# Kernel tuning notes

Hardware: AMD Instinct MI355X
Metric: run time of the kernel (lower is better)

Reference implementation:

```python
import jax, jax.numpy as jnp
import numpy as np

N_NODES = 50000
N_EDGES = 500000
D_NODE = 128
D_EDGE = 128
D_HID = 512
D_OUT = 128


def setup_inputs() -> dict:
    key = jax.random.key(0)
    ks = jax.random.split(key, 6)
    x = jax.random.normal(ks[0], (N_NODES, D_NODE), dtype=jnp.float32)
    edge_index = jax.random.randint(ks[1], (2, N_EDGES), 0, N_NODES, dtype=jnp.int64 if jax.config.jax_enable_x64 else jnp.int32)
    edge_attr = jax.random.normal(ks[2], (N_EDGES, D_EDGE), dtype=jnp.float32)
    cin = 2 * D_NODE + D_EDGE
    W1 = jax.random.normal(ks[3], (cin, D_HID), dtype=jnp.float32) * (1.0 / np.sqrt(cin))
    b1 = jnp.zeros((D_HID,), dtype=jnp.float32)
    W2 = jax.random.normal(ks[4], (D_HID, D_OUT), dtype=jnp.float32) * (1.0 / np.sqrt(D_HID))
    b2 = jnp.zeros((D_OUT,), dtype=jnp.float32)
    return {"x": x, "edge_index": edge_index, "edge_attr": edge_attr,
            "W1": W1, "b1": b1, "W2": W2, "b2": b2}


def reference(x, edge_index, edge_attr, W1, b1, W2, b2):
    row, col = edge_index[0], edge_index[1]
    source = x[row]            # [E, d_node] gather
    target = x[col]            # [E, d_node] gather
    out = jnp.concatenate([source, target, edge_attr], axis=1)  # [E, 2*d_node + d_edge]
    h = jax.nn.relu(out @ W1 + b1)   # [E, d_hid]
    return h @ W2 + b2               # [E, d_out]
```

## Files before the change

kernel.cpp:

```cpp
#include <hip/hip_runtime.h>

#define E_TOTAL 500000
#define N_NODES 50000
#define DN 128
#define CIN 384
#define DH 512
#define DOUT 128
#define MT 128
#define NTILE 3907
#define SA_ROWB 768
#define SH_ROWB 1024
#define SO_LD 132

typedef short short8 __attribute__((ext_vector_type(8)));
typedef float f32x4 __attribute__((ext_vector_type(4)));

__device__ inline short f2bf(float f) {
    unsigned int u = __float_as_uint(f);
    u = (u + 0x7FFFu + ((u >> 16) & 1u)) >> 16;
    return (short)u;
}

__global__ void prep_weights(const float* __restrict__ w1,
                             const float* __restrict__ w2,
                             short* __restrict__ w1t,
                             short* __restrict__ w2t) {
    __shared__ float t[32][33];
    int b = blockIdx.x;
    const float* src; short* dst; int R, C, tr, tc;
    if (b < 192) { src = w1; dst = w1t; R = 384; C = 512; tr = b >> 4; tc = b & 15; }
    else { b -= 192; src = w2; dst = w2t; R = 512; C = 128; tr = b >> 2; tc = b & 3; }
    int lx = threadIdx.x & 31, ly = threadIdx.x >> 5;
#pragma unroll
    for (int p = 0; p < 4; p++) {
        int r = tr * 32 + p * 8 + ly;
        t[p * 8 + ly][lx] = src[(size_t)r * C + tc * 32 + lx];
    }
    __syncthreads();
#pragma unroll
    for (int p = 0; p < 4; p++) {
        int c = tc * 32 + p * 8 + ly;
        dst[(size_t)c * R + tr * 32 + lx] = f2bf(t[lx][p * 8 + ly]);
    }
}

__global__ void cvt_x(const float* __restrict__ x, short* __restrict__ xb) {
    int i = blockIdx.x * 256 + threadIdx.x;
    const float4* s = reinterpret_cast<const float4*>(x) + (size_t)i * 2;
    float4 a = s[0], b = s[1];
    short8 p;
    p[0] = f2bf(a.x); p[1] = f2bf(a.y); p[2] = f2bf(a.z); p[3] = f2bf(a.w);
    p[4] = f2bf(b.x); p[5] = f2bf(b.y); p[6] = f2bf(b.z); p[7] = f2bf(b.w);
    reinterpret_cast<short8*>(xb)[i] = p;
}

__global__ __launch_bounds__(1024, 4) void edge_mlp(
        const short* __restrict__ xb,
        const float* __restrict__ xf,
        const int* __restrict__ ei,
        const float* __restrict__ ea,
        const float* __restrict__ b1,
        const float* __restrict__ b2,
        const short* __restrict__ w1t,
        const short* __restrict__ w2t,
        float* __restrict__ out) {
    __shared__ short sBuf[65536];
    __shared__ int sIdx[2][MT];
    char* sb = (char*)sBuf;

    const int tid = threadIdx.x;
    const int wave = tid >> 6;
    const int lane = tid & 63;
    const int l16 = lane & 15;
    const int quad = lane >> 4;
    const int lane32 = tid & 31;
    const int g = tid >> 5;
    const int xorv = (l16 & 7) << 4;
    const int e0 = blockIdx.x * MT;

    if (tid < 2 * MT) {
        int rr = tid >> 7, r = tid & 127;
        int e = e0 + r; e = e < E_TOTAL ? e : E_TOTAL - 1;
        sIdx[rr][r] = ei[rr * E_TOTAL + e];
    }
    __syncthreads();

    short4 gx[8];
    float4 ge[4];
    if (xb) {
#pragma unroll
        for (int j = 0; j < 4; j++) {
            int r = g + 32 * j;
            gx[j]     = reinterpret_cast<const short4*>(xb + (size_t)sIdx[0][r] * DN)[lane32];
            gx[4 + j] = reinterpret_cast<const short4*>(xb + (size_t)sIdx[1][r] * DN)[lane32];
            int e = e0 + r; e = e < E_TOTAL ? e : E_TOTAL - 1;
            ge[j] = reinterpret_cast<const float4*>(ea + (size_t)e * DN)[lane32];
        }
    } else {
#pragma unroll
        for (int j = 0; j < 4; j++) {
            int r = g + 32 * j;
            float4 v0 = reinterpret_cast<const float4*>(xf + (size_t)sIdx[0][r] * DN)[lane32];
            float4 v1 = reinterpret_cast<const float4*>(xf + (size_t)sIdx[1][r] * DN)[lane32];
            short4 p0, p1;
            p0.x = f2bf(v0.x); p0.y = f2bf(v0.y); p0.z = f2bf(v0.z); p0.w = f2bf(v0.w);
            p1.x = f2bf(v1.x); p1.y = f2bf(v1.y); p1.z = f2bf(v1.z); p1.w = f2bf(v1.w);
            gx[j] = p0; gx[4 + j] = p1;
            int e = e0 + r; e = e < E_TOTAL ? e : E_TOTAL - 1;
            ge[j] = reinterpret_cast<const float4*>(ea + (size_t)e * DN)[lane32];
        }
    }
    const short* base1 = w1t + (size_t)(wave * 32 + l16) * CIN + quad * 8;
    short8 bb[2];
#pragma unroll
    for (int nt = 0; nt < 2; nt++)
        bb[nt] = *reinterpret_cast<const short8*>(base1 + nt * 16 * CIN);
#pragma unroll
    for (int j = 0; j < 4; j++) {
        int r = g + 32 * j;
        int rx = (r & 7) << 4;
        char* row = sb + r * SA_ROWB;
        *reinterpret_cast<short4*>(row + (( 0 * 256 + lane32 * 8) ^ rx)) = gx[j];
        *reinterpret_cast<short4*>(row + (( 1 * 256 + lane32 * 8) ^ rx)) = gx[4 + j];
        short4 p;
        p.x = f2bf(ge[j].x); p.y = f2bf(ge[j].y); p.z = f2bf(ge[j].z); p.w = f2bf(ge[j].w);
        *reinterpret_cast<short4*>(row + (( 2 * 256 + lane32 * 8) ^ rx)) = p;
    }
    __syncthreads();

    f32x4 acc[2][8] = {};
    for (int k = 0; k < CIN; k += 32) {
        short8 bn[2];
        if (k + 32 < CIN) {
#pragma unroll
            for (int nt = 0; nt < 2; nt++)
                bn[nt] = *reinterpret_cast<const short8*>(base1 + nt * 16 * CIN + k + 32);
        }
        short8 a[8];
#pragma unroll
        for (int mt = 0; mt < 8; mt++) {
            int m = mt * 16 + l16;
            a[mt] = *reinterpret_cast<const short8*>(
                sb + m * SA_ROWB + ((2 * k + quad * 16) ^ xorv));
        }
#pragma unroll
        for (int nt = 0; nt < 2; nt++)
#pragma unroll
            for (int mt = 0; mt < 8; mt++)
                acc[nt][mt] = __builtin_amdgcn_mfma_f32_16x16x32_bf16(bb[nt], a[mt], acc[nt][mt], 0, 0, 0);
        if (k + 32 < CIN) {
#pragma unroll
            for (int nt = 0; nt < 2; nt++) bb[nt] = bn[nt];
        }
    }

    const int wn = wave & 7, half = wave >> 3;
    const short* base2 = w2t + (size_t)(wn * 16 + l16) * DH + quad * 8;
    short8 bw = *reinterpret_cast<const short8*>(base2);
    float4 b1v[2];
#pragma unroll
    for (int nt = 0; nt < 2; nt++)
        b1v[nt] = *reinterpret_cast<const float4*>(&b1[wave * 32 + nt * 16 + quad * 4]);

    __syncthreads();

#pragma unroll
    for (int nt = 0; nt < 2; nt++) {
#pragma unroll
        for (int mt = 0; mt < 8; mt++) {
            int m = mt * 16 + l16;
            short4 p;
            p.x = f2bf(fmaxf(acc[nt][mt][0] + b1v[nt].x, 0.0f));
            p.y = f2bf(fmaxf(acc[nt][mt][1] + b1v[nt].y, 0.0f));
            p.z = f2bf(fmaxf(acc[nt][mt][2] + b1v[nt].z, 0.0f));
            p.w = f2bf(fmaxf(acc[nt][mt][3] + b1v[nt].w, 0.0f));
            *reinterpret_cast<short4*>(
                sb + m * SH_ROWB + ((wave * 64 + nt * 32 + quad * 8) ^ xorv)) = p;
        }
    }
    __syncthreads();

    f32x4 acc2[4] = {};
#pragma unroll
    for (int kk = 0; kk < 16; kk++) {
        short8 bn = bw;
        if (kk < 15) bn = *reinterpret_cast<const short8*>(base2 + (kk + 1) * 32);
        short8 hf[4];
#pragma unroll
        for (int mt = 0; mt < 4; mt++) {
            int m = half * 64 + mt * 16 + l16;
            hf[mt] = *reinterpret_cast<const short8*>(
                sb + m * SH_ROWB + ((kk * 64 + quad * 16) ^ xorv));
        }
#pragma unroll
        for (int mt = 0; mt < 4; mt++)
            acc2[mt] = __builtin_amdgcn_mfma_f32_16x16x32_bf16(bw, hf[mt], acc2[mt], 0, 0, 0);
        bw = bn;
    }
    float4 b2v = *reinterpret_cast<const float4*>(&b2[wn * 16 + quad * 4]);
    __syncthreads();

    float (*sO)[SO_LD] = (float (*)[SO_LD])sBuf;
#pragma unroll
    for (int mt = 0; mt < 4; mt++) {
        int m = half * 64 + mt * 16 + l16;
        f32x4 o = acc2[mt];
        float* dst = &sO[m][wn * 16 + quad * 4];
        dst[0] = o[0] + b2v.x; dst[1] = o[1] + b2v.y;
        dst[2] = o[2] + b2v.z; dst[3] = o[3] + b2v.w;
    }
    __syncthreads();
#pragma unroll
    for (int it = 0; it < 4; it++) {
        int idx = tid + it * 1024;
        int row = idx >> 5, col = (idx & 31) * 4;
        int e = e0 + row;
        if (e < E_TOTAL) {
            float4 v = *reinterpret_cast<const float4*>(&sO[row][col]);
            *reinterpret_cast<float4*>(&out[(size_t)e * DOUT + col]) = v;
        }
    }
}

extern "C" void kernel_launch(void* const* d_in, const int* in_sizes, int n_in,
                              void* d_out, int out_size, void* d_ws, size_t ws_size,
                              hipStream_t stream) {
    const float* x  = (const float*)d_in[0];
    const int*   ei = (const int*)d_in[1];
    const float* ea = (const float*)d_in[2];
    const float* W1 = (const float*)d_in[3];
    const float* b1 = (const float*)d_in[4];
    const float* W2 = (const float*)d_in[5];
    const float* b2 = (const float*)d_in[6];
    float* outp = (float*)d_out;

    short* w1t = (short*)d_ws;
    short* w2t = w1t + DH * CIN;
    prep_weights<<<256, 256, 0, stream>>>(W1, W2, w1t, w2t);

    const size_t wt_bytes = (size_t)(DH * CIN + DOUT * DH) * 2;
    const size_t xb_bytes = (size_t)N_NODES * DN * 2;
    short* xbp = nullptr;
    if (ws_size >= wt_bytes + xb_bytes) {
        xbp = w2t + DOUT * DH;
        cvt_x<<<3125, 256, 0, stream>>>(x, xbp);
    }
    edge_mlp<<<NTILE, 1024, 0, stream>>>(xbp, x, ei, ea, b1, b2, w1t, w2t, outp);
}
```

Baseline: 941.7 us.

## Gather node features directly into LDS with global_load_lds and segmented layout

Replaces the register-staged gather of bf16 node rows with direct global-to-LDS loads (global_load_lds, 16 bytes per lane), using a segmented A-tile layout with a pre-swizzled source column so the XOR swizzle is kept. Edge indices are now loaded per lane instead of through a shared index array and a barrier. The weight prep and x conversion kernels are merged into one launch. The aim is to cut register pressure, LDS write instructions and one sync in the gather phase, at the cost of a more intricate layout and a templated duplicate code path.

```diff
diff --git a/kernel.cpp b/kernel.cpp
--- a/kernel.cpp
+++ b/kernel.cpp
@@ -8,7 +8,7 @@
 #define DOUT 128
 #define MT 128
 #define NTILE 3907
-#define SA_ROWB 768
+#define SEG_B 32768
 #define SH_ROWB 1024
 #define SO_LD 132
 
@@ -21,12 +21,30 @@
     return (short)u;
 }
 
-__global__ void prep_weights(const float* __restrict__ w1,
-                             const float* __restrict__ w2,
-                             short* __restrict__ w1t,
-                             short* __restrict__ w2t) {
+__device__ inline void gload16(const void* gsrc, void* ldst) {
+    __builtin_amdgcn_global_load_lds(
+        (const __attribute__((address_space(1))) unsigned int*)gsrc,
+        (__attribute__((address_space(3))) unsigned int*)ldst, 16, 0, 0);
+}
+
+__global__ void prep_all(const float* __restrict__ w1,
+                         const float* __restrict__ w2,
+                         const float* __restrict__ x,
+                         short* __restrict__ w1t,
+                         short* __restrict__ w2t,
+                         short* __restrict__ xb) {
     __shared__ float t[32][33];
     int b = blockIdx.x;
+    if (b >= 256) {
+        int i = (b - 256) * 256 + threadIdx.x;
+        const float4* s = reinterpret_cast<const float4*>(x) + (size_t)i * 2;
+        float4 a = s[0], c = s[1];
+        short8 p;
+        p[0] = f2bf(a.x); p[1] = f2bf(a.y); p[2] = f2bf(a.z); p[3] = f2bf(a.w);
+        p[4] = f2bf(c.x); p[5] = f2bf(c.y); p[6] = f2bf(c.z); p[7] = f2bf(c.w);
+        reinterpret_cast<short8*>(xb)[i] = p;
+        return;
+    }
     const float* src; short* dst; int R, C, tr, tc;
     if (b < 192) { src = w1; dst = w1t; R = 384; C = 512; tr = b >> 4; tc = b & 15; }
     else { b -= 192; src = w2; dst = w2t; R = 512; C = 128; tr = b >> 2; tc = b & 3; }
@@ -44,16 +62,7 @@
     }
 }
 
-__global__ void cvt_x(const float* __restrict__ x, short* __restrict__ xb) {
-    int i = blockIdx.x * 256 + threadIdx.x;
-    const float4* s = reinterpret_cast<const float4*>(x) + (size_t)i * 2;
-    float4 a = s[0], b = s[1];
-    short8 p;
-    p[0] = f2bf(a.x); p[1] = f2bf(a.y); p[2] = f2bf(a.z); p[3] = f2bf(a.w);
-    p[4] = f2bf(b.x); p[5] = f2bf(b.y); p[6] = f2bf(b.z); p[7] = f2bf(b.w);
-    reinterpret_cast<short8*>(xb)[i] = p;
-}
-
+template<int XB>
 __global__ __launch_bounds__(1024, 4) void edge_mlp(
         const short* __restrict__ xb,
         const float* __restrict__ xf,
@@ -65,7 +74,6 @@
         const short* __restrict__ w2t,
         float* __restrict__ out) {
     __shared__ short sBuf[65536];
-    __shared__ int sIdx[2][MT];
     char* sb = (char*)sBuf;
 
     const int tid = threadIdx.x;
@@ -73,151 +81,265 @@
     const int lane = tid & 63;
     const int l16 = lane & 15;
     const int quad = lane >> 4;
-    const int lane32 = tid & 31;
-    const int g = tid >> 5;
     const int xorv = (l16 & 7) << 4;
     const int e0 = blockIdx.x * MT;
 
-    if (tid < 2 * MT) {
-        int rr = tid >> 7, r = tid & 127;
-        int e = e0 + r; e = e < E_TOTAL ? e : E_TOTAL - 1;
-        sIdx[rr][r] = ei[rr * E_TOTAL + e];
-    }
-    __syncthreads();
-
-    short4 gx[8];
-    float4 ge[4];
-    if (xb) {
+    if (XB) {
+        int idxv[4];
 #pragma unroll
         for (int j = 0; j < 4; j++) {
-            int r = g + 32 * j;
-            gx[j]     = reinterpret_cast<const short4*>(xb + (size_t)sIdx[0][r] * DN)[lane32];
-            gx[4 + j] = reinterpret_cast<const short4*>(xb + (size_t)sIdx[1][r] * DN)[lane32];
+            int u = wave + j * 16;
+            int seg = u >> 5;
+            int r4 = (u & 31) * 4;
+            int e = e0 + r4 + (lane >> 4); e = e < E_TOTAL ? e : E_TOTAL - 1;
+            idxv[j] = ei[seg * E_TOTAL + e];
+        }
+        const int lane32 = lane & 31, rsel = lane >> 5;
+        float4 ge[4];
+#pragma unroll
+        for (int j = 0; j < 4; j++) {
+            int r = wave * 8 + j * 2 + rsel;
             int e = e0 + r; e = e < E_TOTAL ? e : E_TOTAL - 1;
             ge[j] = reinterpret_cast<const float4*>(ea + (size_t)e * DN)[lane32];
         }
-    } else {
 #pragma unroll
         for (int j = 0; j < 4; j++) {
-            int r = g + 32 * j;
-            float4 v0 = reinterpret_cast<const float4*>(xf + (size_t)sIdx[0][r] * DN)[lane32];
-            float4 v1 = reinterpret_cast<const float4*>(xf + (size_t)sIdx[1][r] * DN)[lane32];
-            short4 p0, p1;
-            p0.x = f2bf(v0.x); p0.y = f2bf(v0.y); p0.z = f2bf(v0.z); p0.w = f2bf(v0.w);
-            p1.x = f2bf(v1.x); p1.y = f2bf(v1.y); p1.z = f2bf(v1.z); p1.w = f2bf(v1.w);
-            gx[j] = p0; gx[4 + j] = p1;
-            int e = e0 + r; e = e < E_TOTAL ? e : E_TOTAL - 1;
-            ge[j] = reinterpret_cast<const float4*>(ea + (size_t)e * DN)[lane32];
-        }
-    }
-    const short* base1 = w1t + (size_t)(wave * 32 + l16) * CIN + quad * 8;
-    short8 bb[2];
-#pragma unroll
-    for (int nt = 0; nt < 2; nt++)
-        bb[nt] = *reinterpret_cast<const short8*>(base1 + nt * 16 * CIN);
-#pragma unroll
-    for (int j = 0; j < 4; j++) {
-        int r = g + 32 * j;
-        int rx = (r & 7) << 4;
-        char* row = sb + r * SA_ROWB;
-        *reinterpret_cast<short4*>(row + (( 0 * 256 + lane32 * 8) ^ rx)) = gx[j];
-        *reinterpret_cast<short4*>(row + (( 1 * 256 + lane32 * 8) ^ rx)) = gx[4 + j];
-        short4 p;
-        p.x = f2bf(ge[j].x); p.y = f2bf(ge[j].y); p.z = f2bf(ge[j].z); p.w = f2bf(ge[j].w);
-        *reinterpret_cast<short4*>(row + (( 2 * 256 + lane32 * 8) ^ rx)) = p;
-    }
-    __syncthreads();
-
-    f32x4 acc[2][8] = {};
-    for (int k = 0; k < CIN; k += 32) {
-        short8 bn[2];
-        if (k + 32 < CIN) {
+            int u = wave + j * 16;
+            int seg = u >> 5;
+            int r4 = (u & 31) * 4;
+            int row = r4 + (lane >> 4);
+            int lc = ((lane & 15) * 16) ^ ((row & 7) << 4);
+            const char* gsrc = (const char*)(xb + (size_t)idxv[j] * DN) + lc;
+            gload16(gsrc, sb + seg * SEG_B + r4 * 256);
+        }
+        const short* base1p = w1t + (size_t)(wave * 32 + l16) * CIN + quad * 8;
+        short8 bb0 = *reinterpret_cast<const short8*>(base1p);
+        short8 bb1 = *reinterpret_cast<const short8*>(base1p + 16 * CIN);
+#pragma unroll
+        for (int j = 0; j < 4; j++) {
+            int r = wave * 8 + j * 2 + rsel;
+            short4 p;
+            p.x = f2bf(ge[j].x); p.y = f2bf(ge[j].y); p.z = f2bf(ge[j].z); p.w = f2bf(ge[j].w);
+            int pc = (lane32 * 8) ^ ((r & 7) << 4);
+            *reinterpret_cast<short4*>(sb + 2 * SEG_B + r * 256 + pc) = p;
+        }
+        __syncthreads();
+
+        f32x4 acc[2][8] = {};
+        short8 bb[2] = {bb0, bb1};
+        for (int k = 0; k < CIN; k += 32) {
+            short8 bn[2];
+            if (k + 32 < CIN) {
+#pragma unroll
+                for (int nt = 0; nt < 2; nt++)
+                    bn[nt] = *reinterpret_cast<const short8*>(base1p + nt * 16 * CIN + k + 32);
+            }
+            int segb = (k >> 7) * SEG_B, kk2 = 2 * (k & 127);
+            short8 a[8];
+#pragma unroll
+            for (int mt = 0; mt < 8; mt++) {
+                int m = mt * 16 + l16;
+                a[mt] = *reinterpret_cast<const short8*>(
+                    sb + segb + m * 256 + ((kk2 + quad * 16) ^ xorv));
+            }
 #pragma unroll
             for (int nt = 0; nt < 2; nt++)
-                bn[nt] = *reinterpret_cast<const short8*>(base1 + nt * 16 * CIN + k + 32);
-        }
-        short8 a[8];
-#pragma unroll
-        for (int mt = 0; mt < 8; mt++) {
-            int m = mt * 16 + l16;
-            a[mt] = *reinterpret_cast<const short8*>(
-                sb + m * SA_ROWB + ((2 * k + quad * 16) ^ xorv));
-        }
+#pragma unroll
+                for (int mt = 0; mt < 8; mt++)
+                    acc[nt][mt] = __builtin_amdgcn_mfma_f32_16x16x32_bf16(bb[nt], a[mt], acc[nt][mt], 0, 0, 0);
+            if (k + 32 < CIN) { bb[0] = bn[0]; bb[1] = bn[1]; }
+        }
+
+        const int wn = wave & 7, half = wave >> 3;
+        const short* base2 = w2t + (size_t)(wn * 16 + l16) * DH + quad * 8;
+        short8 bw = *reinterpret_cast<const short8*>(base2);
+        float4 b1v[2];
 #pragma unroll
         for (int nt = 0; nt < 2; nt++)
-#pragma unroll
-            for (int mt = 0; mt < 8; mt++)
-                acc[nt][mt] = __builtin_amdgcn_mfma_f32_16x16x32_bf16(bb[nt], a[mt], acc[nt][mt], 0, 0, 0);
-        if (k + 32 < CIN) {
-#pragma unroll
-            for (int nt = 0; nt < 2; nt++) bb[nt] = bn[nt];
-        }
-    }
-
-    const int wn = wave & 7, half = wave >> 3;
-    const short* base2 = w2t + (size_t)(wn * 16 + l16) * DH + quad * 8;
-    short8 bw = *reinterpret_cast<const short8*>(base2);
-    float4 b1v[2];
-#pragma unroll
-    for (int nt = 0; nt < 2; nt++)
-        b1v[nt] = *reinterpret_cast<const float4*>(&b1[wave * 32 + nt * 16 + quad * 4]);
-
-    __syncthreads();
-
-#pragma unroll
-    for (int nt = 0; nt < 2; nt++) {
-#pragma unroll
-        for (int mt = 0; mt < 8; mt++) {
-            int m = mt * 16 + l16;
-            short4 p;
-            p.x = f2bf(fmaxf(acc[nt][mt][0] + b1v[nt].x, 0.0f));
-            p.y = f2bf(fmaxf(acc[nt][mt][1] + b1v[nt].y, 0.0f));
-            p.z = f2bf(fmaxf(acc[nt][mt][2] + b1v[nt].z, 0.0f));
-            p.w = f2bf(fmaxf(acc[nt][mt][3] + b1v[nt].w, 0.0f));
-            *reinterpret_cast<short4*>(
-                sb + m * SH_ROWB + ((wave * 64 + nt * 32 + quad * 8) ^ xorv)) = p;
-        }
-    }
-    __syncthreads();
-
-    f32x4 acc2[4] = {};
-#pragma unroll
-    for (int kk = 0; kk < 16; kk++) {
-        short8 bn = bw;
-        if (kk < 15) bn = *reinterpret_cast<const short8*>(base2 + (kk + 1) * 32);
-        short8 hf[4];
+            b1v[nt] = *reinterpret_cast<const float4*>(&b1[wave * 32 + nt * 16 + quad * 4]);
+        __syncthreads();
+
+#pragma unroll
+        for (int nt = 0; nt < 2; nt++) {
+#pragma unroll
+            for (int mt = 0; mt < 8; mt++) {
+                int m = mt * 16 + l16;
+                short4 p;
+                p.x = f2bf(fmaxf(acc[nt][mt][0] + b1v[nt].x, 0.0f));
+                p.y = f2bf(fmaxf(acc[nt][mt][1] + b1v[nt].y, 0.0f));
+                p.z = f2bf(fmaxf(acc[nt][mt][2] + b1v[nt].z, 0.0f));
+                p.w = f2bf(fmaxf(acc[nt][mt][3] + b1v[nt].w, 0.0f));
+                *reinterpret_cast<short4*>(
+                    sb + m * SH_ROWB + ((wave * 64 + nt * 32 + quad * 8) ^ xorv)) = p;
+            }
+        }
+        __syncthreads();
+
+        f32x4 acc2[4] = {};
+#pragma unroll
+        for (int kk = 0; kk < 16; kk++) {
+            short8 bn = bw;
+            if (kk < 15) bn = *reinterpret_cast<const short8*>(base2 + (kk + 1) * 32);
+            short8 hf[4];
+#pragma unroll
+            for (int mt = 0; mt < 4; mt++) {
+                int m = half * 64 + mt * 16 + l16;
+                hf[mt] = *reinterpret_cast<const short8*>(
+                    sb + m * SH_ROWB + ((kk * 64 + quad * 16) ^ xorv));
+            }
+#pragma unroll
+            for (int mt = 0; mt < 4; mt++)
+                acc2[mt] = __builtin_amdgcn_mfma_f32_16x16x32_bf16(bw, hf[mt], acc2[mt], 0, 0, 0);
+            bw = bn;
+        }
+        float4 b2v = *reinterpret_cast<const float4*>(&b2[wn * 16 + quad * 4]);
+        __syncthreads();
+
+        float (*sO)[SO_LD] = (float (*)[SO_LD])sBuf;
 #pragma unroll
         for (int mt = 0; mt < 4; mt++) {
             int m = half * 64 + mt * 16 + l16;
-            hf[mt] = *reinterpret_cast<const short8*>(
-                sb + m * SH_ROWB + ((kk * 64 + quad * 16) ^ xorv));
-        }
-#pragma unroll
-        for (int mt = 0; mt < 4; mt++)
-            acc2[mt] = __builtin_amdgcn_mfma_f32_16x16x32_bf16(bw, hf[mt], acc2[mt], 0, 0, 0);
-        bw = bn;
-    }
-    float4 b2v = *reinterpret_cast<const float4*>(&b2[wn * 16 + quad * 4]);
-    __syncthreads();
-
-    float (*sO)[SO_LD] = (float (*)[SO_LD])sBuf;
-#pragma unroll
-    for (int mt = 0; mt < 4; mt++) {
-        int m = half * 64 + mt * 16 + l16;
-        f32x4 o = acc2[mt];
-        float* dst = &sO[m][wn * 16 + quad * 4];
-        dst[0] = o[0] + b2v.x; dst[1] = o[1] + b2v.y;
-        dst[2] = o[2] + b2v.z; dst[3] = o[3] + b2v.w;
-    }
-    __syncthreads();
-#pragma unroll
-    for (int it = 0; it < 4; it++) {
-        int idx = tid + it * 1024;
-        int row = idx >> 5, col = (idx & 31) * 4;
-        int e = e0 + row;
-        if (e < E_TOTAL) {
-            float4 v = *reinterpret_cast<const float4*>(&sO[row][col]);
-            *reinterpret_cast<float4*>(&out[(size_t)e * DOUT + col]) = v;
+            float* dst = &sO[m][wn * 16 + quad * 4];
+            dst[0] = acc2[mt][0] + b2v.x; dst[1] = acc2[mt][1] + b2v.y;
+            dst[2] = acc2[mt][2] + b2v.z; dst[3] = acc2[mt][3] + b2v.w;
+        }
+        __syncthreads();
+#pragma unroll
+        for (int it = 0; it < 4; it++) {
+            int idx = tid + it * 1024;
+            int row = idx >> 5, col = (idx & 31) * 4;
+            int e = e0 + row;
+            if (e < E_TOTAL) {
+                float4 v = *reinterpret_cast<const float4*>(&sO[row][col]);
+                *reinterpret_cast<float4*>(&out[(size_t)e * DOUT + col]) = v;
+            }
+        }
+    } else {
+        int* sIdx = (int*)(sb + 122880);
+        if (tid < 2 * MT) {
+            int rr = tid >> 7, r = tid & 127;
+            int e = e0 + r; e = e < E_TOTAL ? e : E_TOTAL - 1;
+            sIdx[rr * MT + r] = ei[rr * E_TOTAL + e];
+        }
+        __syncthreads();
+        const int lane32 = lane & 31;
+        const int g = tid >> 5;
+#pragma unroll
+        for (int h2 = 0; h2 < 2; h2++) {
+            float4 v0[2], v1[2], ve[2];
+#pragma unroll
+            for (int jj = 0; jj < 2; jj++) {
+                int r = g + 32 * (h2 * 2 + jj);
+                v0[jj] = reinterpret_cast<const float4*>(xf + (size_t)sIdx[r] * DN)[lane32];
+                v1[jj] = reinterpret_cast<const float4*>(xf + (size_t)sIdx[MT + r] * DN)[lane32];
+                int e = e0 + r; e = e < E_TOTAL ? e : E_TOTAL - 1;
+                ve[jj] = reinterpret_cast<const float4*>(ea + (size_t)e * DN)[lane32];
+            }
+#pragma unroll
+            for (int jj = 0; jj < 2; jj++) {
+                int r = g + 32 * (h2 * 2 + jj);
+                int rx = (r & 7) << 4;
+                int pc0 = (lane32 & 15) * 16 + (lane32 >> 4) * 8;
+                (void)pc0;
+                int pc = (lane32 * 8) ^ rx;
+                short4 p0, p1, pe;
+                p0.x = f2bf(v0[jj].x); p0.y = f2bf(v0[jj].y); p0.z = f2bf(v0[jj].z); p0.w = f2bf(v0[jj].w);
+                p1.x = f2bf(v1[jj].x); p1.y = f2bf(v1[jj].y); p1.z = f2bf(v1[jj].z); p1.w = f2bf(v1[jj].w);
+                pe.x = f2bf(ve[jj].x); pe.y = f2bf(ve[jj].y); pe.z = f2bf(ve[jj].z); pe.w = f2bf(ve[jj].w);
+                *reinterpret_cast<short4*>(sb + 0 * SEG_B + r * 256 + pc) = p0;
+                *reinterpret_cast<short4*>(sb + 1 * SEG_B + r * 256 + pc) = p1;
+                *reinterpret_cast<short4*>(sb + 2 * SEG_B + r * 256 + pc) = pe;
+            }
+        }
+        const short* base1p = w1t + (size_t)(wave * 32 + l16) * CIN + quad * 8;
+        short8 bb0 = *reinterpret_cast<const short8*>(base1p);
+        short8 bb1 = *reinterpret_cast<const short8*>(base1p + 16 * CIN);
+        __syncthreads();
+
+        f32x4 acc[2][8] = {};
+        short8 bb[2] = {bb0, bb1};
+        for (int k = 0; k < CIN; k += 32) {
+            short8 bn[2];
+            if (k + 32 < CIN) {
+#pragma unroll
+                for (int nt = 0; nt < 2; nt++)
+                    bn[nt] = *reinterpret_cast<const short8*>(base1p + nt * 16 * CIN + k + 32);
+            }
+            int segb = (k >> 7) * SEG_B, kk2 = 2 * (k & 127);
+            short8 a[8];
+#pragma unroll
+            for (int mt = 0; mt < 8; mt++) {
+                int m = mt * 16 + l16;
+                a[mt] = *reinterpret_cast<const short8*>(
+                    sb + segb + m * 256 + ((kk2 + quad * 16) ^ xorv));
+            }
+#pragma unroll
+            for (int nt = 0; nt < 2; nt++)
+#pragma unroll
+                for (int mt = 0; mt < 8; mt++)
+                    acc[nt][mt] = __builtin_amdgcn_mfma_f32_16x16x32_bf16(bb[nt], a[mt], acc[nt][mt], 0, 0, 0);
+            if (k + 32 < CIN) { bb[0] = bn[0]; bb[1] = bn[1]; }
+        }
+        const int wn = wave & 7, half = wave >> 3;
+        const short* base2 = w2t + (size_t)(wn * 16 + l16) * DH + quad * 8;
+        short8 bw = *reinterpret_cast<const short8*>(base2);
+        float4 b1v[2];
+#pragma unroll
+        for (int nt = 0; nt < 2; nt++)
+            b1v[nt] = *reinterpret_cast<const float4*>(&b1[wave * 32 + nt * 16 + quad * 4]);
+        __syncthreads();
+#pragma unroll
+        for (int nt = 0; nt < 2; nt++) {
+#pragma unroll
+            for (int mt = 0; mt < 8; mt++) {
+                int m = mt * 16 + l16;
+                short4 p;
+                p.x = f2bf(fmaxf(acc[nt][mt][0] + b1v[nt].x, 0.0f));
+                p.y = f2bf(fmaxf(acc[nt][mt][1] + b1v[nt].y, 0.0f));
+                p.z = f2bf(fmaxf(acc[nt][mt][2] + b1v[nt].z, 0.0f));
+                p.w = f2bf(fmaxf(acc[nt][mt][3] + b1v[nt].w, 0.0f));
+                *reinterpret_cast<short4*>(
+                    sb + m * SH_ROWB + ((wave * 64 + nt * 32 + quad * 8) ^ xorv)) = p;
+            }
+        }
+        __syncthreads();
+        f32x4 acc2[4] = {};
+#pragma unroll
+        for (int kk = 0; kk < 16; kk++) {
+            short8 bn = bw;
+            if (kk < 15) bn = *reinterpret_cast<const short8*>(base2 + (kk + 1) * 32);
+            short8 hf[4];
+#pragma unroll
+            for (int mt = 0; mt < 4; mt++) {
+                int m = half * 64 + mt * 16 + l16;
+                hf[mt] = *reinterpret_cast<const short8*>(
+                    sb + m * SH_ROWB + ((kk * 64 + quad * 16) ^ xorv));
+            }
+#pragma unroll
+            for (int mt = 0; mt < 4; mt++)
+                acc2[mt] = __builtin_amdgcn_mfma_f32_16x16x32_bf16(bw, hf[mt], acc2[mt], 0, 0, 0);
+            bw = bn;
+        }
+        float4 b2v = *reinterpret_cast<const float4*>(&b2[wn * 16 + quad * 4]);
+        __syncthreads();
+        float (*sO)[SO_LD] = (float (*)[SO_LD])sBuf;
+#pragma unroll
+        for (int mt = 0; mt < 4; mt++) {
+            int m = half * 64 + mt * 16 + l16;
+            float* dst = &sO[m][wn * 16 + quad * 4];
+            dst[0] = acc2[mt][0] + b2v.x; dst[1] = acc2[mt][1] + b2v.y;
+            dst[2] = acc2[mt][2] + b2v.z; dst[3] = acc2[mt][3] + b2v.w;
+        }
+        __syncthreads();
+#pragma unroll
+        for (int it = 0; it < 4; it++) {
+            int idx = tid + it * 1024;
+            int row = idx >> 5, col = (idx & 31) * 4;
+            int e = e0 + row;
+            if (e < E_TOTAL) {
+                float4 v = *reinterpret_cast<const float4*>(&sO[row][col]);
+                *reinterpret_cast<float4*>(&out[(size_t)e * DOUT + col]) = v;
+            }
         }
     }
 }
@@ -236,14 +358,16 @@
 
     short* w1t = (short*)d_ws;
     short* w2t = w1t + DH * CIN;
-    prep_weights<<<256, 256, 0, stream>>>(W1, W2, w1t, w2t);
 
     const size_t wt_bytes = (size_t)(DH * CIN + DOUT * DH) * 2;
     const size_t xb_bytes = (size_t)N_NODES * DN * 2;
-    short* xbp = nullptr;
-    if (ws_size >= wt_bytes + xb_bytes) {
-        xbp = w2t + DOUT * DH;
-        cvt_x<<<3125, 256, 0, stream>>>(x, xbp);
-    }
-    edge_mlp<<<NTILE, 1024, 0, stream>>>(xbp, x, ei, ea, b1, b2, w1t, w2t, outp);
-}
+    const bool has_xb = ws_size >= wt_bytes + xb_bytes;
+    short* xbp = has_xb ? (w2t + DOUT * DH) : nullptr;
+
+    prep_all<<<has_xb ? 3381 : 256, 256, 0, stream>>>(W1, W2, x, w1t, w2t, xbp);
+
+    if (has_xb)
+        edge_mlp<1><<<NTILE, 1024, 0, stream>>>(xbp, x, ei, ea, b1, b2, w1t, w2t, outp);
+    else
+        edge_mlp<0><<<NTILE, 1024, 0, stream>>>(nullptr, x, ei, ea, b1, b2, w1t, w2t, outp);
+}
```

After: 872.7 us. 1.08x faster.

## Make edge MLP persistent with double-buffered async gather of next tile

Applied to the files above, without the earlier changes.

Switches the edge MLP to a persistent kernel with 256 blocks of 64-edge tiles. While the current tile runs its MFMAs, the next tile's node rows are prefetched into a second LDS buffer with global_load_lds, and its edge attributes are held in registers. Weight prep and x conversion are merged into one launch. The aim is to hide gather latency behind compute and cut launch overhead, at the cost of smaller tiles, more LDS per block (lower occupancy) and only 256 blocks on the GPU.

```diff
diff --git a/kernel.cpp b/kernel.cpp
--- a/kernel.cpp
+++ b/kernel.cpp
@@ -6,10 +6,12 @@
 #define CIN 384
 #define DH 512
 #define DOUT 128
-#define MT 128
-#define NTILE 3907
-#define SA_ROWB 768
-#define SH_ROWB 1024
+#define MT 64
+#define NTILE 7813
+#define NPERS 256
+#define SEG_B 16384
+#define ABUF_B 49152
+#define SH_OFF 98304
 #define SO_LD 132
 
 typedef short short8 __attribute__((ext_vector_type(8)));
@@ -21,12 +23,36 @@
     return (short)u;
 }
 
-__global__ void prep_weights(const float* __restrict__ w1,
-                             const float* __restrict__ w2,
-                             short* __restrict__ w1t,
-                             short* __restrict__ w2t) {
+__device__ inline void gload16(const void* gsrc, void* ldst) {
+    __builtin_amdgcn_global_load_lds(
+        (const __attribute__((address_space(1))) unsigned int*)gsrc,
+        (__attribute__((address_space(3))) unsigned int*)ldst, 16, 0, 0);
+}
+
+__device__ inline short4 cvt4(float4 v) {
+    short4 p;
+    p.x = f2bf(v.x); p.y = f2bf(v.y); p.z = f2bf(v.z); p.w = f2bf(v.w);
+    return p;
+}
+
+__global__ void prep_all(const float* __restrict__ w1,
+                         const float* __restrict__ w2,
+                         const float* __restrict__ x,
+                         short* __restrict__ w1t,
+                         short* __restrict__ w2t,
+                         short* __restrict__ xb) {
     __shared__ float t[32][33];
     int b = blockIdx.x;
+    if (b >= 256) {
+        int i = (b - 256) * 256 + threadIdx.x;
+        const float4* s = reinterpret_cast<const float4*>(x) + (size_t)i * 2;
+        float4 a = s[0], c = s[1];
+        short8 p;
+        p[0] = f2bf(a.x); p[1] = f2bf(a.y); p[2] = f2bf(a.z); p[3] = f2bf(a.w);
+        p[4] = f2bf(c.x); p[5] = f2bf(c.y); p[6] = f2bf(c.z); p[7] = f2bf(c.w);
+        reinterpret_cast<short8*>(xb)[i] = p;
+        return;
+    }
     const float* src; short* dst; int R, C, tr, tc;
     if (b < 192) { src = w1; dst = w1t; R = 384; C = 512; tr = b >> 4; tc = b & 15; }
     else { b -= 192; src = w2; dst = w2t; R = 512; C = 128; tr = b >> 2; tc = b & 3; }
@@ -44,16 +70,7 @@
     }
 }
 
-__global__ void cvt_x(const float* __restrict__ x, short* __restrict__ xb) {
-    int i = blockIdx.x * 256 + threadIdx.x;
-    const float4* s = reinterpret_cast<const float4*>(x) + (size_t)i * 2;
-    float4 a = s[0], b = s[1];
-    short8 p;
-    p[0] = f2bf(a.x); p[1] = f2bf(a.y); p[2] = f2bf(a.z); p[3] = f2bf(a.w);
-    p[4] = f2bf(b.x); p[5] = f2bf(b.y); p[6] = f2bf(b.z); p[7] = f2bf(b.w);
-    reinterpret_cast<short8*>(xb)[i] = p;
-}
-
+template<bool XB>
 __global__ __launch_bounds__(1024, 4) void edge_mlp(
         const short* __restrict__ xb,
         const float* __restrict__ xf,
@@ -64,8 +81,7 @@
         const short* __restrict__ w1t,
         const short* __restrict__ w2t,
         float* __restrict__ out) {
-    __shared__ short sBuf[65536];
-    __shared__ int sIdx[2][MT];
+    __shared__ short sBuf[81920];
     char* sb = (char*)sBuf;
 
     const int tid = threadIdx.x;
@@ -73,152 +89,189 @@
     const int lane = tid & 63;
     const int l16 = lane & 15;
     const int quad = lane >> 4;
-    const int lane32 = tid & 31;
-    const int g = tid >> 5;
     const int xorv = (l16 & 7) << 4;
-    const int e0 = blockIdx.x * MT;
-
-    if (tid < 2 * MT) {
-        int rr = tid >> 7, r = tid & 127;
-        int e = e0 + r; e = e < E_TOTAL ? e : E_TOTAL - 1;
-        sIdx[rr][r] = ei[rr * E_TOTAL + e];
-    }
-    __syncthreads();
-
-    short4 gx[8];
-    float4 ge[4];
-    if (xb) {
-#pragma unroll
-        for (int j = 0; j < 4; j++) {
-            int r = g + 32 * j;
-            gx[j]     = reinterpret_cast<const short4*>(xb + (size_t)sIdx[0][r] * DN)[lane32];
-            gx[4 + j] = reinterpret_cast<const short4*>(xb + (size_t)sIdx[1][r] * DN)[lane32];
-            int e = e0 + r; e = e < E_TOTAL ? e : E_TOTAL - 1;
-            ge[j] = reinterpret_cast<const float4*>(ea + (size_t)e * DN)[lane32];
-        }
-    } else {
-#pragma unroll
-        for (int j = 0; j < 4; j++) {
-            int r = g + 32 * j;
-            float4 v0 = reinterpret_cast<const float4*>(xf + (size_t)sIdx[0][r] * DN)[lane32];
-            float4 v1 = reinterpret_cast<const float4*>(xf + (size_t)sIdx[1][r] * DN)[lane32];
-            short4 p0, p1;
-            p0.x = f2bf(v0.x); p0.y = f2bf(v0.y); p0.z = f2bf(v0.z); p0.w = f2bf(v0.w);
-            p1.x = f2bf(v1.x); p1.y = f2bf(v1.y); p1.z = f2bf(v1.z); p1.w = f2bf(v1.w);
-            gx[j] = p0; gx[4 + j] = p1;
-            int e = e0 + r; e = e < E_TOTAL ? e : E_TOTAL - 1;
-            ge[j] = reinterpret_cast<const float4*>(ea + (size_t)e * DN)[lane32];
-        }
-    }
+
     const short* base1 = w1t + (size_t)(wave * 32 + l16) * CIN + quad * 8;
-    short8 bb[2];
-#pragma unroll
-    for (int nt = 0; nt < 2; nt++)
-        bb[nt] = *reinterpret_cast<const short8*>(base1 + nt * 16 * CIN);
-#pragma unroll
-    for (int j = 0; j < 4; j++) {
-        int r = g + 32 * j;
-        int rx = (r & 7) << 4;
-        char* row = sb + r * SA_ROWB;
-        *reinterpret_cast<short4*>(row + (( 0 * 256 + lane32 * 8) ^ rx)) = gx[j];
-        *reinterpret_cast<short4*>(row + (( 1 * 256 + lane32 * 8) ^ rx)) = gx[4 + j];
-        short4 p;
-        p.x = f2bf(ge[j].x); p.y = f2bf(ge[j].y); p.z = f2bf(ge[j].z); p.w = f2bf(ge[j].w);
-        *reinterpret_cast<short4*>(row + (( 2 * 256 + lane32 * 8) ^ rx)) = p;
-    }
-    __syncthreads();
-
-    f32x4 acc[2][8] = {};
-    for (int k = 0; k < CIN; k += 32) {
-        short8 bn[2];
-        if (k + 32 < CIN) {
-#pragma unroll
-            for (int nt = 0; nt < 2; nt++)
-                bn[nt] = *reinterpret_cast<const short8*>(base1 + nt * 16 * CIN + k + 32);
-        }
-        short8 a[8];
-#pragma unroll
-        for (int mt = 0; mt < 8; mt++) {
-            int m = mt * 16 + l16;
-            a[mt] = *reinterpret_cast<const short8*>(
-                sb + m * SA_ROWB + ((2 * k + quad * 16) ^ xorv));
-        }
-#pragma unroll
-        for (int nt = 0; nt < 2; nt++)
-#pragma unroll
-            for (int mt = 0; mt < 8; mt++)
-                acc[nt][mt] = __builtin_amdgcn_mfma_f32_16x16x32_bf16(bb[nt], a[mt], acc[nt][mt], 0, 0, 0);
-        if (k + 32 < CIN) {
-#pragma unroll
-            for (int nt = 0; nt < 2; nt++) bb[nt] = bn[nt];
-        }
-    }
-
     const int wn = wave & 7, half = wave >> 3;
     const short* base2 = w2t + (size_t)(wn * 16 + l16) * DH + quad * 8;
-    short8 bw = *reinterpret_cast<const short8*>(base2);
     float4 b1v[2];
 #pragma unroll
     for (int nt = 0; nt < 2; nt++)
         b1v[nt] = *reinterpret_cast<const float4*>(&b1[wave * 32 + nt * 16 + quad * 4]);
-
-    __syncthreads();
-
-#pragma unroll
-    for (int nt = 0; nt < 2; nt++) {
-#pragma unroll
-        for (int mt = 0; mt < 8; mt++) {
-            int m = mt * 16 + l16;
-            short4 p;
-            p.x = f2bf(fmaxf(acc[nt][mt][0] + b1v[nt].x, 0.0f));
-            p.y = f2bf(fmaxf(acc[nt][mt][1] + b1v[nt].y, 0.0f));
-            p.z = f2bf(fmaxf(acc[nt][mt][2] + b1v[nt].z, 0.0f));
-            p.w = f2bf(fmaxf(acc[nt][mt][3] + b1v[nt].w, 0.0f));
-            *reinterpret_cast<short4*>(
-                sb + m * SH_ROWB + ((wave * 64 + nt * 32 + quad * 8) ^ xorv)) = p;
-        }
-    }
-    __syncthreads();
-
-    f32x4 acc2[4] = {};
-#pragma unroll
-    for (int kk = 0; kk < 16; kk++) {
-        short8 bn = bw;
-        if (kk < 15) bn = *reinterpret_cast<const short8*>(base2 + (kk + 1) * 32);
-        short8 hf[4];
-#pragma unroll
-        for (int mt = 0; mt < 4; mt++) {
-            int m = half * 64 + mt * 16 + l16;
-            hf[mt] = *reinterpret_cast<const short8*>(
-                sb + m * SH_ROWB + ((kk * 64 + quad * 16) ^ xorv));
-        }
-#pragma unroll
-        for (int mt = 0; mt < 4; mt++)
-            acc2[mt] = __builtin_amdgcn_mfma_f32_16x16x32_bf16(bw, hf[mt], acc2[mt], 0, 0, 0);
-        bw = bn;
-    }
     float4 b2v = *reinterpret_cast<const float4*>(&b2[wn * 16 + quad * 4]);
-    __syncthreads();
-
-    float (*sO)[SO_LD] = (float (*)[SO_LD])sBuf;
-#pragma unroll
-    for (int mt = 0; mt < 4; mt++) {
-        int m = half * 64 + mt * 16 + l16;
-        f32x4 o = acc2[mt];
-        float* dst = &sO[m][wn * 16 + quad * 4];
-        dst[0] = o[0] + b2v.x; dst[1] = o[1] + b2v.y;
-        dst[2] = o[2] + b2v.z; dst[3] = o[3] + b2v.w;
-    }
-    __syncthreads();
-#pragma unroll
-    for (int it = 0; it < 4; it++) {
-        int idx = tid + it * 1024;
-        int row = idx >> 5, col = (idx & 31) * 4;
-        int e = e0 + row;
-        if (e < E_TOTAL) {
-            float4 v = *reinterpret_cast<const float4*>(&sO[row][col]);
-            *reinterpret_cast<float4*>(&out[(size_t)e * DOUT + col]) = v;
-        }
+
+    const int grow = wave * 4 + (lane >> 4);
+    const int grx = (grow & 7) << 4;
+
+    int t = blockIdx.x;
+    int cur = 0;
+
+    {
+        int e = t * MT + grow; e = e < E_TOTAL ? e : E_TOTAL - 1;
+        if (XB) {
+#pragma unroll
+            for (int s = 0; s < 2; s++) {
+                int idx = ei[s * E_TOTAL + e];
+                int lc = (l16 * 16) ^ grx;
+                gload16((const char*)(xb + (size_t)idx * DN) + lc,
+                        sb + s * SEG_B + wave * 1024);
+            }
+        } else {
+#pragma unroll
+            for (int s = 0; s < 2; s++) {
+                int idx = ei[s * E_TOTAL + e];
+                const float4* xp = reinterpret_cast<const float4*>(xf + (size_t)idx * DN);
+                float4 fa = xp[l16], fb = xp[l16 + 16];
+                char* seg = sb + s * SEG_B + grow * 256;
+                *reinterpret_cast<short4*>(seg + ((l16 * 8) ^ grx)) = cvt4(fa);
+                *reinterpret_cast<short4*>(seg + ((l16 * 8 + 128) ^ grx)) = cvt4(fb);
+            }
+        }
+        const float4* ep = reinterpret_cast<const float4*>(ea + (size_t)e * DN);
+        float4 fa = ep[l16], fb = ep[l16 + 16];
+        char* seg2 = sb + 2 * SEG_B + grow * 256;
+        *reinterpret_cast<short4*>(seg2 + ((l16 * 8) ^ grx)) = cvt4(fa);
+        *reinterpret_cast<short4*>(seg2 + ((l16 * 8 + 128) ^ grx)) = cvt4(fb);
+        __syncthreads();
+    }
+
+#pragma unroll 1
+    for (;;) {
+        const int tn = t + NPERS;
+        const bool hasN = tn < NTILE;
+        const int nxt = cur ^ 1;
+        char* curA = sb + cur * ABUF_B;
+        char* nxtA = sb + nxt * ABUF_B;
+
+        float4 efa, efb;
+        float4 xga[2], xgb[2];
+        if (hasN) {
+            int e = tn * MT + grow; e = e < E_TOTAL ? e : E_TOTAL - 1;
+            if (XB) {
+#pragma unroll
+                for (int s = 0; s < 2; s++) {
+                    int idx = ei[s * E_TOTAL + e];
+                    int lc = (l16 * 16) ^ grx;
+                    gload16((const char*)(xb + (size_t)idx * DN) + lc,
+                            nxtA + s * SEG_B + wave * 1024);
+                }
+            } else {
+#pragma unroll
+                for (int s = 0; s < 2; s++) {
+                    int idx = ei[s * E_TOTAL + e];
+                    const float4* xp = reinterpret_cast<const float4*>(xf + (size_t)idx * DN);
+                    xga[s] = xp[l16]; xgb[s] = xp[l16 + 16];
+                }
+            }
+            const float4* ep = reinterpret_cast<const float4*>(ea + (size_t)e * DN);
+            efa = ep[l16]; efb = ep[l16 + 16];
+        }
+
+        f32x4 acc[2][4] = {};
+        {
+            short8 bb[2];
+            bb[0] = *reinterpret_cast<const short8*>(base1);
+            bb[1] = *reinterpret_cast<const short8*>(base1 + 16 * CIN);
+            for (int k = 0; k < CIN; k += 32) {
+                short8 bn[2];
+                if (k + 32 < CIN) {
+                    bn[0] = *reinterpret_cast<const short8*>(base1 + k + 32);
+                    bn[1] = *reinterpret_cast<const short8*>(base1 + 16 * CIN + k + 32);
+                }
+                const char* abase = curA + (k >> 7) * SEG_B;
+                const int ko = 2 * (k & 127);
+                short8 a[4];
+#pragma unroll
+                for (int mt = 0; mt < 4; mt++) {
+                    int m = mt * 16 + l16;
+                    a[mt] = *reinterpret_cast<const short8*>(
+                        abase + m * 256 + ((ko + quad * 16) ^ xorv));
+                }
+#pragma unroll
+                for (int nt = 0; nt < 2; nt++)
+#pragma unroll
+                    for (int mt = 0; mt < 4; mt++)
+                        acc[nt][mt] = __builtin_amdgcn_mfma_f32_16x16x32_bf16(bb[nt], a[mt], acc[nt][mt], 0, 0, 0);
+                if (k + 32 < CIN) { bb[0] = bn[0]; bb[1] = bn[1]; }
+            }
+        }
+
+#pragma unroll
+        for (int nt = 0; nt < 2; nt++) {
+#pragma unroll
+            for (int mt = 0; mt < 4; mt++) {
+                int m = mt * 16 + l16;
+                float4 v;
+                v.x = fmaxf(acc[nt][mt][0] + b1v[nt].x, 0.0f);
+                v.y = fmaxf(acc[nt][mt][1] + b1v[nt].y, 0.0f);
+                v.z = fmaxf(acc[nt][mt][2] + b1v[nt].z, 0.0f);
+                v.w = fmaxf(acc[nt][mt][3] + b1v[nt].w, 0.0f);
+                *reinterpret_cast<short4*>(
+                    sb + SH_OFF + m * 1024 + ((wave * 64 + nt * 32 + quad * 8) ^ xorv)) = cvt4(v);
+            }
+        }
+        __syncthreads();
+
+        f32x4 acc2[2] = {};
+        {
+            short8 bw = *reinterpret_cast<const short8*>(base2);
+#pragma unroll
+            for (int kk = 0; kk < 16; kk++) {
+                short8 bnx = bw;
+                if (kk < 15) bnx = *reinterpret_cast<const short8*>(base2 + (kk + 1) * 32);
+                short8 hf[2];
+#pragma unroll
+                for (int mt = 0; mt < 2; mt++) {
+                    int m = half * 32 + mt * 16 + l16;
+                    hf[mt] = *reinterpret_cast<const short8*>(
+                        sb + SH_OFF + m * 1024 + ((kk * 64 + quad * 16) ^ xorv));
+                }
+#pragma unroll
+                for (int mt = 0; mt < 2; mt++)
+                    acc2[mt] = __builtin_amdgcn_mfma_f32_16x16x32_bf16(bw, hf[mt], acc2[mt], 0, 0, 0);
+                bw = bnx;
+            }
+        }
+        __syncthreads();
+
+        float* sO = (float*)(sb + SH_OFF);
+#pragma unroll
+        for (int mt = 0; mt < 2; mt++) {
+            int m = half * 32 + mt * 16 + l16;
+            float* dst = sO + m * SO_LD + wn * 16 + quad * 4;
+            dst[0] = acc2[mt][0] + b2v.x; dst[1] = acc2[mt][1] + b2v.y;
+            dst[2] = acc2[mt][2] + b2v.z; dst[3] = acc2[mt][3] + b2v.w;
+        }
+        __syncthreads();
+#pragma unroll
+        for (int it = 0; it < 2; it++) {
+            int idx = tid + it * 1024;
+            int row = idx >> 5, c4 = (idx & 31) * 4;
+            int e = t * MT + row;
+            if (e < E_TOTAL) {
+                float4 v = *reinterpret_cast<const float4*>(sO + row * SO_LD + c4);
+                *reinterpret_cast<float4*>(&out[(size_t)e * DOUT + c4]) = v;
+            }
+        }
+
+        if (!hasN) break;
+
+        {
+            char* seg2 = nxtA + 2 * SEG_B + grow * 256;
+            *reinterpret_cast<short4*>(seg2 + ((l16 * 8) ^ grx)) = cvt4(efa);
+            *reinterpret_cast<short4*>(seg2 + ((l16 * 8 + 128) ^ grx)) = cvt4(efb);
+            if (!XB) {
+#pragma unroll
+                for (int s = 0; s < 2; s++) {
+                    char* seg = nxtA + s * SEG_B + grow * 256;
+                    *reinterpret_cast<short4*>(seg + ((l16 * 8) ^ grx)) = cvt4(xga[s]);
+                    *reinterpret_cast<short4*>(seg + ((l16 * 8 + 128) ^ grx)) = cvt4(xgb[s]);
+                }
+            }
+        }
+        __syncthreads();
+
+        cur = nxt; t = tn;
     }
 }
 
@@ -236,14 +289,16 @@
 
     short* w1t = (short*)d_ws;
     short* w2t = w1t + DH * CIN;
-    prep_weights<<<256, 256, 0, stream>>>(W1, W2, w1t, w2t);
 
     const size_t wt_bytes = (size_t)(DH * CIN + DOUT * DH) * 2;
     const size_t xb_bytes = (size_t)N_NODES * DN * 2;
-    short* xbp = nullptr;
-    if (ws_size >= wt_bytes + xb_bytes) {
-        xbp = w2t + DOUT * DH;
-        cvt_x<<<3125, 256, 0, stream>>>(x, xbp);
-    }
-    edge_mlp<<<NTILE, 1024, 0, stream>>>(xbp, x, ei, ea, b1, b2, w1t, w2t, outp);
-}
+    const bool has_xb = ws_size >= wt_bytes + xb_bytes;
+    short* xbp = has_xb ? (w2t + DOUT * DH) : nullptr;
+
+    prep_all<<<has_xb ? 3381 : 256, 256, 0, stream>>>(W1, W2, x, w1t, w2t, xbp);
+
+    if (has_xb)
+        edge_mlp<true><<<NPERS, 1024, 0, stream>>>(xbp, x, ei, ea, b1, b2, w1t, w2t, outp);
+    else
+        edge_mlp<false><<<NPERS, 1024, 0, stream>>>(nullptr, x, ei, ea, b1, b2, w1t, w2t, outp);
+}
```

Result: slower. 1.144 ms (+21.5%).
